# Optimization experiments

Hardware: AMD Instinct MI355X
Metric: run time of the kernel (lower is better)

## Reference

```python
import jax, jax.numpy as jnp
import numpy as np

N, K, D = 32768, 8192, 64  # active voxels, codebook size, embedding dim


def setup_inputs() -> dict:
    key = jax.random.key(0)
    k1, k2 = jax.random.split(key)
    z_feats = jax.random.normal(k1, (N, D), dtype=jnp.float32)
    codebook = jax.random.normal(k2, (K, D), dtype=jnp.float32)  # nn.Embedding weight, N(0,1)
    return {"z_feats": z_feats, "codebook": codebook}


def reference(z_feats, codebook):
    # torch.cdist(z, E) followed by argmin(dim=1). sqrt is monotonic, so argmin over
    # squared Euclidean distances gives identical indices (same math, cheaper).
    # d2[n,k] = ||z_n||^2 - 2 z_n . e_k + ||e_k||^2  -> [N, K] (dominant intermediate)
    d2 = (jnp.sum(z_feats * z_feats, axis=1, keepdims=True)
          - 2.0 * (z_feats @ codebook.T)
          + jnp.sum(codebook * codebook, axis=1))
    encoding_indices = jnp.argmin(d2, axis=1)  # [N]

    quantized_feats = codebook[encoding_indices]  # embedding gather [N, D]

    # F.mse_loss == mean over all elements
    commitment_loss = jnp.mean((z_feats - jax.lax.stop_gradient(quantized_feats)) ** 2)
    vq_loss = jnp.mean((quantized_feats - jax.lax.stop_gradient(z_feats)) ** 2)

    # straight-through estimator
    quantized = z_feats + jax.lax.stop_gradient(quantized_feats - z_feats)
    return quantized, vq_loss, commitment_loss, encoding_indices
```

## Files before the change

### kernel.cpp

```cpp
#include <hip/hip_runtime.h>
#include <cfloat>


typedef __bf16 bf16x8 __attribute__((ext_vector_type(8)));
typedef float  f32x16 __attribute__((ext_vector_type(16)));

constexpr int N_ROWS = 32768;
constexpr int K_CB   = 8192;
constexpr int D_DIM  = 64;
constexpr size_t NQ  = (size_t)N_ROWS * D_DIM;
constexpr int WS_LOSS = K_CB;
constexpr size_t WS_SPLIT_F   = 8448;
constexpr size_t SPLIT_BYTES  = (size_t)K_CB * D_DIM * 4;
constexpr size_t WS_NEED      = WS_SPLIT_F * 4 + SPLIT_BYTES;
constexpr int NROUND = K_CB / 256;

__global__ __launch_bounds__(256) void vq_prep(const float* __restrict__ cb,
                                               float* __restrict__ ws) {
  const int k = blockIdx.x * 256 + threadIdx.x;
  if (k == 0) ws[WS_LOSS] = 0.0f;
  const float4* p = reinterpret_cast<const float4*>(cb) + (size_t)k * 16;
  float s0 = 0.f, s1 = 0.f, s2 = 0.f, s3 = 0.f;
#pragma unroll
  for (int j = 0; j < 16; ++j) {
    float4 v = p[j];
    s0 = fmaf(v.x, v.x, s0); s1 = fmaf(v.y, v.y, s1);
    s2 = fmaf(v.z, v.z, s2); s3 = fmaf(v.w, v.w, s3);
  }
  ws[k] = -0.5f * ((s0 + s1) + (s2 + s3));
}

__global__ __launch_bounds__(256) void vq_split(const float* __restrict__ cb,
                                                float* __restrict__ ws) {
  const int u  = blockIdx.x * 256 + threadIdx.x;
  const int k  = u >> 3, ch = u & 7;
  const int r  = k >> 8, t = (k >> 5) & 7, c = k & 31;
  const float* src = cb + (size_t)k * D_DIM + ch * 8;
  float4 f0 = *reinterpret_cast<const float4*>(src);
  float4 f1 = *reinterpret_cast<const float4*>(src + 4);
  float xs[8] = {f0.x, f0.y, f0.z, f0.w, f1.x, f1.y, f1.z, f1.w};
  bf16x8 hi, lo;
#pragma unroll
  for (int j = 0; j < 8; ++j) {
    __bf16 h = (__bf16)xs[j];
    hi[j] = h;
    lo[j] = (__bf16)(xs[j] - (float)h);
  }
  char* base = reinterpret_cast<char*>(ws + WS_SPLIT_F) +
               (size_t)r * 65536 + (size_t)t * 8192 + (size_t)ch * 512 + (size_t)c * 16;
  *reinterpret_cast<bf16x8*>(base)        = hi;
  *reinterpret_cast<bf16x8*>(base + 4096) = lo;
}

__global__ __launch_bounds__(512, 2) void vq_gd2(const float* __restrict__ z,
                                                 const float* __restrict__ cb,
                                                 float* __restrict__ ws,
                                                 float* __restrict__ out) {
  __shared__ __attribute__((aligned(16))) unsigned char lds[12288];

  const int tid = threadIdx.x;
  const int w = tid >> 6, l = tid & 63;
  const int c = l & 31, g = l >> 5;
  const int rowbase = blockIdx.x * 128;

  bf16x8 zh[4][4], zl[4][4];
#pragma unroll
  for (int q = 0; q < 4; ++q) {
    const float* zr = z + (size_t)(rowbase + q * 32 + c) * D_DIM + 8 * g;
#pragma unroll
    for (int s = 0; s < 4; ++s) {
      float4 f0 = *reinterpret_cast<const float4*>(zr + 16 * s);
      float4 f1 = *reinterpret_cast<const float4*>(zr + 16 * s + 4);
      float xs[8] = {f0.x, f0.y, f0.z, f0.w, f1.x, f1.y, f1.z, f1.w};
#pragma unroll
      for (int j = 0; j < 8; ++j) {
        __bf16 h = (__bf16)xs[j];
        zh[q][s][j] = h;
        zl[q][s][j] = (__bf16)(xs[j] - (float)h);
      }
    }
  }

  const char* hp = reinterpret_cast<const char*>(ws + WS_SPLIT_F) +
                   (size_t)w * 8192 + (size_t)g * 512 + (size_t)c * 16;
  const char* lq = hp + 4096;
  const float* rp = ws + w * 32 + 4 * g;

  bf16x8 fh[4], fl[4];
#pragma unroll
  for (int s = 0; s < 4; ++s) {
    fh[s] = *reinterpret_cast<const bf16x8*>(hp + s * 1024);
    fl[s] = *reinterpret_cast<const bf16x8*>(lq + s * 1024);
  }
  float4 rv0 = *reinterpret_cast<const float4*>(rp);
  float4 rv1 = *reinterpret_cast<const float4*>(rp + 8);
  float4 rv2 = *reinterpret_cast<const float4*>(rp + 16);
  float4 rv3 = *reinterpret_cast<const float4*>(rp + 24);

  float gbest[4];
  int   bpack[4];
#pragma unroll
  for (int q = 0; q < 4; ++q) { gbest[q] = -FLT_MAX; bpack[q] = 0; }

  for (int r = 0; r < NROUND; ++r) {
    f32x16 ainit;
    ainit[0] = rv0.x; ainit[1] = rv0.y; ainit[2]  = rv0.z; ainit[3]  = rv0.w;
    ainit[4] = rv1.x; ainit[5] = rv1.y; ainit[6]  = rv1.z; ainit[7]  = rv1.w;
    ainit[8] = rv2.x; ainit[9] = rv2.y; ainit[10] = rv2.z; ainit[11] = rv2.w;
    ainit[12] = rv3.x; ainit[13] = rv3.y; ainit[14] = rv3.z; ainit[15] = rv3.w;
    f32x16 a0 = ainit, a1 = ainit, a2 = ainit, a3 = ainit;

    __builtin_amdgcn_s_setprio(1);
#pragma unroll
    for (int s = 0; s < 4; ++s) {
      a0 = __builtin_amdgcn_mfma_f32_32x32x16_bf16(fh[s], zh[0][s], a0, 0, 0, 0);
      a1 = __builtin_amdgcn_mfma_f32_32x32x16_bf16(fh[s], zh[1][s], a1, 0, 0, 0);
      a2 = __builtin_amdgcn_mfma_f32_32x32x16_bf16(fh[s], zh[2][s], a2, 0, 0, 0);
      a3 = __builtin_amdgcn_mfma_f32_32x32x16_bf16(fh[s], zh[3][s], a3, 0, 0, 0);
      a0 = __builtin_amdgcn_mfma_f32_32x32x16_bf16(fh[s], zl[0][s], a0, 0, 0, 0);
      a1 = __builtin_amdgcn_mfma_f32_32x32x16_bf16(fh[s], zl[1][s], a1, 0, 0, 0);
      a2 = __builtin_amdgcn_mfma_f32_32x32x16_bf16(fh[s], zl[2][s], a2, 0, 0, 0);
      a3 = __builtin_amdgcn_mfma_f32_32x32x16_bf16(fh[s], zl[3][s], a3, 0, 0, 0);
      a0 = __builtin_amdgcn_mfma_f32_32x32x16_bf16(fl[s], zh[0][s], a0, 0, 0, 0);
      a1 = __builtin_amdgcn_mfma_f32_32x32x16_bf16(fl[s], zh[1][s], a1, 0, 0, 0);
      a2 = __builtin_amdgcn_mfma_f32_32x32x16_bf16(fl[s], zh[2][s], a2, 0, 0, 0);
      a3 = __builtin_amdgcn_mfma_f32_32x32x16_bf16(fl[s], zh[3][s], a3, 0, 0, 0);
    }
    __builtin_amdgcn_s_setprio(0);

    if (r < NROUND - 1) {
      hp += 65536; lq += 65536; rp += 256;
#pragma unroll
      for (int s = 0; s < 4; ++s) {
        fh[s] = *reinterpret_cast<const bf16x8*>(hp + s * 1024);
        fl[s] = *reinterpret_cast<const bf16x8*>(lq + s * 1024);
      }
      rv0 = *reinterpret_cast<const float4*>(rp);
      rv1 = *reinterpret_cast<const float4*>(rp + 8);
      rv2 = *reinterpret_cast<const float4*>(rp + 16);
      rv3 = *reinterpret_cast<const float4*>(rp + 24);
    }

    const int pb = r << 4;
#pragma unroll
    for (int q = 0; q < 4; ++q) {
      const f32x16& a = (q == 0) ? a0 : (q == 1) ? a1 : (q == 2) ? a2 : a3;
      float m = a[0];
#pragma unroll
      for (int i = 1; i < 16; ++i) m = fmaxf(m, a[i]);
      int bi = 0;
#pragma unroll
      for (int i = 15; i >= 0; --i) bi = (a[i] == m) ? i : bi;
      bool upd = m > gbest[q];
      gbest[q] = upd ? m : gbest[q];
      bpack[q] = upd ? (pb + bi) : bpack[q];
    }
  }

  int bk[4];
#pragma unroll
  for (int q = 0; q < 4; ++q) {
    int rr = bpack[q] >> 4, i = bpack[q] & 15;
    int cid = (i & 3) + 8 * (i >> 2) + 4 * g;
    bk[q] = rr * 256 + w * 32 + cid;
  }
#pragma unroll
  for (int q = 0; q < 4; ++q) {
    float ob = __shfl_xor(gbest[q], 32, 64);
    int   ok = __shfl_xor(bk[q], 32, 64);
    if (ob > gbest[q] || (ob == gbest[q] && ok < bk[q])) { gbest[q] = ob; bk[q] = ok; }
  }

  float* fbuf = reinterpret_cast<float*>(lds);
  int*   kbuf = reinterpret_cast<int*>(lds + 4096);
  int*   ibuf = reinterpret_cast<int*>(lds + 8192);
  if (l < 32) {
#pragma unroll
    for (int q = 0; q < 4; ++q) {
      fbuf[w * 128 + q * 32 + l] = gbest[q];
      kbuf[w * 128 + q * 32 + l] = bk[q];
    }
  }
  __syncthreads();

  if (tid < 128) {
    float bb = fbuf[tid];
    int   kk = kbuf[tid];
#pragma unroll
    for (int ww = 1; ww < 8; ++ww) {
      float b2 = fbuf[ww * 128 + tid];
      int   k2 = kbuf[ww * 128 + tid];
      if (b2 > bb || (b2 == bb && k2 < kk)) { bb = b2; kk = k2; }
    }
    ibuf[tid] = kk;
    out[NQ + 2 + rowbase + tid] = (float)kk;
  }
  __syncthreads();

  {
    const int row_l = tid >> 2, seg = tid & 3;
    const int idx  = ibuf[row_l];
    const int grow = rowbase + row_l;
    const float4* qp = reinterpret_cast<const float4*>(cb + (size_t)idx * D_DIM + seg * 16);
    const float4* zp = reinterpret_cast<const float4*>(z + (size_t)grow * D_DIM + seg * 16);
    float4*       op = reinterpret_cast<float4*>(out + (size_t)grow * D_DIM + seg * 16);
    float lp = 0.f;
#pragma unroll
    for (int cc = 0; cc < 4; ++cc) {
      float4 qv = qp[cc], zv = zp[cc];
      op[cc] = qv;
      float dx = zv.x - qv.x, dy = zv.y - qv.y;
      float dz = zv.z - qv.z, dw = zv.w - qv.w;
      lp += (dx * dx + dy * dy) + (dz * dz + dw * dw);
    }
#pragma unroll
    for (int off = 32; off > 0; off >>= 1) lp += __shfl_down(lp, off, 64);
    if (l == 0) atomicAdd(ws + WS_LOSS, lp);
  }
}

__global__ __launch_bounds__(512, 2) void vq_main_reg(const float* __restrict__ z,
                                                      const float* __restrict__ cb,
                                                      float* __restrict__ ws,
                                                      float* __restrict__ out) {
  __shared__ __attribute__((aligned(16))) unsigned char lds[65536];
  const int tid = threadIdx.x;
  const int w = tid >> 6, l = tid & 63;
  const int rg = w >> 1, sp = w & 1;
  const int c = l & 31, g = l >> 5;
  const int rowbase = blockIdx.x * 128;
  const int myrow = rowbase + rg * 32 + c;

  bf16x8 zh[4], zl[4];
#pragma unroll
  for (int s = 0; s < 4; ++s) {
    const float* zp = z + (size_t)myrow * D_DIM + 16 * s + 8 * g;
    float4 f0 = *reinterpret_cast<const float4*>(zp);
    float4 f1 = *reinterpret_cast<const float4*>(zp + 4);
    float xs[8] = {f0.x, f0.y, f0.z, f0.w, f1.x, f1.y, f1.z, f1.w};
#pragma unroll
    for (int j = 0; j < 8; ++j) {
      __bf16 h = (__bf16)xs[j];
      zh[s][j] = h; zl[s][j] = (__bf16)(xs[j] - (float)h);
    }
  }
  const int st_t01 = tid >> 8;
  const int st_c   = (tid >> 3) & 31;
  const int st_ch  = tid & 7;
  const unsigned st_off = (unsigned)(st_t01 * 16384 + st_ch * 512 + st_c * 16);
  const float* st_g = cb + (size_t)(st_t01 * 32 + st_c) * D_DIM + st_ch * 8;

  float best = -FLT_MAX;
  int   bidx = 0;
  float4 p0 = *reinterpret_cast<const float4*>(st_g);
  float4 p1 = *reinterpret_cast<const float4*>(st_g + 4);
  {
    float xs[8] = {p0.x, p0.y, p0.z, p0.w, p1.x, p1.y, p1.z, p1.w};
    bf16x8 hi, lo;
#pragma unroll
    for (int j = 0; j < 8; ++j) {
      __bf16 h = (__bf16)xs[j];
      hi[j] = h; lo[j] = (__bf16)(xs[j] - (float)h);
    }
    *reinterpret_cast<bf16x8*>(lds + st_off)        = hi;
    *reinterpret_cast<bf16x8*>(lds + st_off + 8192) = lo;
  }
  __syncthreads();
  const unsigned rd_base = (unsigned)(sp * 16384 + c * 16);
  for (int r = 0; r < 128; ++r) {
    const int buf = r & 1;
    if (r < 127) {
      const float* gp = st_g + (size_t)(r + 1) * (64 * D_DIM);
      p0 = *reinterpret_cast<const float4*>(gp);
      p1 = *reinterpret_cast<const float4*>(gp + 4);
    }
    const unsigned b0 = (unsigned)buf * 32768u + rd_base;
    bf16x8 ch[4], cl[4];
#pragma unroll
    for (int s = 0; s < 4; ++s) {
      unsigned off = b0 + (unsigned)((2 * s + g) * 512);
      ch[s] = *reinterpret_cast<const bf16x8*>(lds + off);
      cl[s] = *reinterpret_cast<const bf16x8*>(lds + off + 8192);
    }
    f32x16 acc;
#pragma unroll
    for (int i = 0; i < 16; ++i) acc[i] = 0.f;
#pragma unroll
    for (int s = 0; s < 4; ++s) {
      acc = __builtin_amdgcn_mfma_f32_32x32x16_bf16(ch[s], zh[s], acc, 0, 0, 0);
      acc = __builtin_amdgcn_mfma_f32_32x32x16_bf16(ch[s], zl[s], acc, 0, 0, 0);
      acc = __builtin_amdgcn_mfma_f32_32x32x16_bf16(cl[s], zh[s], acc, 0, 0, 0);
    }
    const int tb = (2 * r + sp) * 32 + 4 * g;
#pragma unroll
    for (int q = 0; q < 4; ++q) {
      float4 rv = *reinterpret_cast<const float4*>(ws + tb + 8 * q);
      float ra[4] = {rv.x, rv.y, rv.z, rv.w};
#pragma unroll
      for (int j = 0; j < 4; ++j) {
        float sc = ra[j] + acc[4 * q + j];
        int kg = tb + 8 * q + j;
        if (sc > best) { best = sc; bidx = kg; }
      }
    }
    if (r < 127) {
      float xs[8] = {p0.x, p0.y, p0.z, p0.w, p1.x, p1.y, p1.z, p1.w};
      bf16x8 hi, lo;
#pragma unroll
      for (int j = 0; j < 8; ++j) {
        __bf16 h = (__bf16)xs[j];
        hi[j] = h; lo[j] = (__bf16)(xs[j] - (float)h);
      }
      unsigned wo = (unsigned)(buf ^ 1) * 32768u + st_off;
      *reinterpret_cast<bf16x8*>(lds + wo)        = hi;
      *reinterpret_cast<bf16x8*>(lds + wo + 8192) = lo;
    }
    __syncthreads();
  }
  {
    float ob = __shfl_xor(best, 32, 64);
    int   oi = __shfl_xor(bidx, 32, 64);
    if (ob > best || (ob == best && oi < bidx)) { best = ob; bidx = oi; }
  }
  float* mf  = reinterpret_cast<float*>(lds);
  int*   mi  = reinterpret_cast<int*>(lds + 1024);
  int*   mix = reinterpret_cast<int*>(lds + 2048);
  if (l < 32) { mf[w * 32 + c] = best; mi[w * 32 + c] = bidx; }
  __syncthreads();
  if (tid < 128) {
    int rgg = tid >> 5, rl = tid & 31;
    float b0 = mf[(2 * rgg) * 32 + rl];     int i0 = mi[(2 * rgg) * 32 + rl];
    float b1 = mf[(2 * rgg + 1) * 32 + rl]; int i1 = mi[(2 * rgg + 1) * 32 + rl];
    int idx = (b1 > b0 || (b1 == b0 && i1 < i0)) ? i1 : i0;
    mix[tid] = idx;
    out[NQ + 2 + rowbase + tid] = (float)idx;
  }
  __syncthreads();
  {
    const int row_l = tid >> 2, seg = tid & 3;
    const int idx  = mix[row_l];
    const int grow = rowbase + row_l;
    const float4* qp = reinterpret_cast<const float4*>(cb + (size_t)idx * D_DIM + seg * 16);
    const float4* zp = reinterpret_cast<const float4*>(z + (size_t)grow * D_DIM + seg * 16);
    float4*       op = reinterpret_cast<float4*>(out + (size_t)grow * D_DIM + seg * 16);
    float lp = 0.f;
#pragma unroll
    for (int cc = 0; cc < 4; ++cc) {
      float4 qv = qp[cc], zv = zp[cc];
      op[cc] = qv;
      float dx = zv.x - qv.x, dy = zv.y - qv.y;
      float dz = zv.z - qv.z, dw = zv.w - qv.w;
      lp += (dx * dx + dy * dy) + (dz * dz + dw * dw);
    }
#pragma unroll
    for (int off = 32; off > 0; off >>= 1) lp += __shfl_down(lp, off, 64);
    if (l == 0) atomicAdd(ws + WS_LOSS, lp);
  }
}

__global__ void vq_fin(const float* __restrict__ ws, float* __restrict__ out) {
  float mm = ws[WS_LOSS] * (1.0f / (float)(N_ROWS * D_DIM));
  out[NQ]     = mm;
  out[NQ + 1] = mm;
}

extern "C" void kernel_launch(void* const* d_in, const int* in_sizes, int n_in,
                              void* d_out, int out_size, void* d_ws, size_t ws_size,
                              hipStream_t stream) {
  (void)in_sizes; (void)n_in; (void)out_size;
  const float* z  = (const float*)d_in[0];
  const float* cb = (const float*)d_in[1];
  float* out = (float*)d_out;
  float* ws  = (float*)d_ws;

  vq_prep<<<K_CB / 256, 256, 0, stream>>>(cb, ws);
  if (ws_size >= WS_NEED) {
    vq_split<<<256, 256, 0, stream>>>(cb, ws);
    vq_gd2<<<N_ROWS / 128, 512, 0, stream>>>(z, cb, ws, out);
  } else {
    vq_main_reg<<<N_ROWS / 128, 512, 0, stream>>>(z, cb, ws, out);
  }
  vq_fin<<<1, 1, 0, stream>>>(ws, out);
}
```

Measured before the change: 129.4 us.

## Halve rows per block to raise occupancy in VQ distance kernel

The fused distance/argmin kernel now processes 64 rows per block instead of 128, keeping two MFMA accumulators per wave and launching twice as many blocks with a min-blocks hint of 4. Lower register pressure and a larger grid are meant to improve latency hiding and CU fill. In exchange, each codebook fragment loaded from global memory is reused across half as many rows, doubling codebook read traffic. The epilogue reduction and gather are resized to match.

```diff
diff --git a/kernel.cpp b/kernel.cpp
--- a/kernel.cpp
+++ b/kernel.cpp
@@ -52,20 +52,20 @@
   *reinterpret_cast<bf16x8*>(base + 4096) = lo;
 }
 
-__global__ __launch_bounds__(512, 2) void vq_gd2(const float* __restrict__ z,
+__global__ __launch_bounds__(512, 4) void vq_gd3(const float* __restrict__ z,
                                                  const float* __restrict__ cb,
                                                  float* __restrict__ ws,
                                                  float* __restrict__ out) {
-  __shared__ __attribute__((aligned(16))) unsigned char lds[12288];
+  __shared__ __attribute__((aligned(16))) unsigned char lds[8192];
 
   const int tid = threadIdx.x;
   const int w = tid >> 6, l = tid & 63;
   const int c = l & 31, g = l >> 5;
-  const int rowbase = blockIdx.x * 128;
-
-  bf16x8 zh[4][4], zl[4][4];
-#pragma unroll
-  for (int q = 0; q < 4; ++q) {
+  const int rowbase = blockIdx.x * 64;
+
+  bf16x8 zh[2][4], zl[2][4];
+#pragma unroll
+  for (int q = 0; q < 2; ++q) {
     const float* zr = z + (size_t)(rowbase + q * 32 + c) * D_DIM + 8 * g;
 #pragma unroll
     for (int s = 0; s < 4; ++s) {
@@ -97,34 +97,26 @@
   float4 rv2 = *reinterpret_cast<const float4*>(rp + 16);
   float4 rv3 = *reinterpret_cast<const float4*>(rp + 24);
 
-  float gbest[4];
-  int   bpack[4];
-#pragma unroll
-  for (int q = 0; q < 4; ++q) { gbest[q] = -FLT_MAX; bpack[q] = 0; }
+  float gbest0 = -FLT_MAX, gbest1 = -FLT_MAX;
+  int   bp0 = 0, bp1 = 0;
 
   for (int r = 0; r < NROUND; ++r) {
     f32x16 ainit;
-    ainit[0] = rv0.x; ainit[1] = rv0.y; ainit[2]  = rv0.z; ainit[3]  = rv0.w;
-    ainit[4] = rv1.x; ainit[5] = rv1.y; ainit[6]  = rv1.z; ainit[7]  = rv1.w;
-    ainit[8] = rv2.x; ainit[9] = rv2.y; ainit[10] = rv2.z; ainit[11] = rv2.w;
+    ainit[0]  = rv0.x; ainit[1]  = rv0.y; ainit[2]  = rv0.z; ainit[3]  = rv0.w;
+    ainit[4]  = rv1.x; ainit[5]  = rv1.y; ainit[6]  = rv1.z; ainit[7]  = rv1.w;
+    ainit[8]  = rv2.x; ainit[9]  = rv2.y; ainit[10] = rv2.z; ainit[11] = rv2.w;
     ainit[12] = rv3.x; ainit[13] = rv3.y; ainit[14] = rv3.z; ainit[15] = rv3.w;
-    f32x16 a0 = ainit, a1 = ainit, a2 = ainit, a3 = ainit;
+    f32x16 a0 = ainit, a1 = ainit;
 
     __builtin_amdgcn_s_setprio(1);
 #pragma unroll
     for (int s = 0; s < 4; ++s) {
       a0 = __builtin_amdgcn_mfma_f32_32x32x16_bf16(fh[s], zh[0][s], a0, 0, 0, 0);
       a1 = __builtin_amdgcn_mfma_f32_32x32x16_bf16(fh[s], zh[1][s], a1, 0, 0, 0);
-      a2 = __builtin_amdgcn_mfma_f32_32x32x16_bf16(fh[s], zh[2][s], a2, 0, 0, 0);
-      a3 = __builtin_amdgcn_mfma_f32_32x32x16_bf16(fh[s], zh[3][s], a3, 0, 0, 0);
       a0 = __builtin_amdgcn_mfma_f32_32x32x16_bf16(fh[s], zl[0][s], a0, 0, 0, 0);
       a1 = __builtin_amdgcn_mfma_f32_32x32x16_bf16(fh[s], zl[1][s], a1, 0, 0, 0);
-      a2 = __builtin_amdgcn_mfma_f32_32x32x16_bf16(fh[s], zl[2][s], a2, 0, 0, 0);
-      a3 = __builtin_amdgcn_mfma_f32_32x32x16_bf16(fh[s], zl[3][s], a3, 0, 0, 0);
       a0 = __builtin_amdgcn_mfma_f32_32x32x16_bf16(fl[s], zh[0][s], a0, 0, 0, 0);
       a1 = __builtin_amdgcn_mfma_f32_32x32x16_bf16(fl[s], zh[1][s], a1, 0, 0, 0);
-      a2 = __builtin_amdgcn_mfma_f32_32x32x16_bf16(fl[s], zh[2][s], a2, 0, 0, 0);
-      a3 = __builtin_amdgcn_mfma_f32_32x32x16_bf16(fl[s], zh[3][s], a3, 0, 0, 0);
     }
     __builtin_amdgcn_s_setprio(0);
 
@@ -142,54 +134,62 @@
     }
 
     const int pb = r << 4;
-#pragma unroll
-    for (int q = 0; q < 4; ++q) {
-      const f32x16& a = (q == 0) ? a0 : (q == 1) ? a1 : (q == 2) ? a2 : a3;
-      float m = a[0];
-#pragma unroll
-      for (int i = 1; i < 16; ++i) m = fmaxf(m, a[i]);
+    {
+      float m = a0[0];
+#pragma unroll
+      for (int i = 1; i < 16; ++i) m = fmaxf(m, a0[i]);
       int bi = 0;
 #pragma unroll
-      for (int i = 15; i >= 0; --i) bi = (a[i] == m) ? i : bi;
-      bool upd = m > gbest[q];
-      gbest[q] = upd ? m : gbest[q];
-      bpack[q] = upd ? (pb + bi) : bpack[q];
-    }
-  }
-
-  int bk[4];
-#pragma unroll
-  for (int q = 0; q < 4; ++q) {
-    int rr = bpack[q] >> 4, i = bpack[q] & 15;
-    int cid = (i & 3) + 8 * (i >> 2) + 4 * g;
-    bk[q] = rr * 256 + w * 32 + cid;
-  }
-#pragma unroll
-  for (int q = 0; q < 4; ++q) {
-    float ob = __shfl_xor(gbest[q], 32, 64);
-    int   ok = __shfl_xor(bk[q], 32, 64);
-    if (ob > gbest[q] || (ob == gbest[q] && ok < bk[q])) { gbest[q] = ob; bk[q] = ok; }
+      for (int i = 15; i >= 0; --i) bi = (a0[i] == m) ? i : bi;
+      bool upd = m > gbest0;
+      gbest0 = upd ? m : gbest0;
+      bp0    = upd ? (pb + bi) : bp0;
+    }
+    {
+      float m = a1[0];
+#pragma unroll
+      for (int i = 1; i < 16; ++i) m = fmaxf(m, a1[i]);
+      int bi = 0;
+#pragma unroll
+      for (int i = 15; i >= 0; --i) bi = (a1[i] == m) ? i : bi;
+      bool upd = m > gbest1;
+      gbest1 = upd ? m : gbest1;
+      bp1    = upd ? (pb + bi) : bp1;
+    }
+  }
+
+  int bk0, bk1;
+  {
+    int rr = bp0 >> 4, i = bp0 & 15;
+    bk0 = rr * 256 + w * 32 + (i & 3) + 8 * (i >> 2) + 4 * g;
+    rr = bp1 >> 4; i = bp1 & 15;
+    bk1 = rr * 256 + w * 32 + (i & 3) + 8 * (i >> 2) + 4 * g;
+  }
+  {
+    float ob = __shfl_xor(gbest0, 32, 64);
+    int   ok = __shfl_xor(bk0, 32, 64);
+    if (ob > gbest0 || (ob == gbest0 && ok < bk0)) { gbest0 = ob; bk0 = ok; }
+    ob = __shfl_xor(gbest1, 32, 64);
+    ok = __shfl_xor(bk1, 32, 64);
+    if (ob > gbest1 || (ob == gbest1 && ok < bk1)) { gbest1 = ob; bk1 = ok; }
   }
 
   float* fbuf = reinterpret_cast<float*>(lds);
-  int*   kbuf = reinterpret_cast<int*>(lds + 4096);
-  int*   ibuf = reinterpret_cast<int*>(lds + 8192);
+  int*   kbuf = reinterpret_cast<int*>(lds + 2048);
+  int*   ibuf = reinterpret_cast<int*>(lds + 4096);
   if (l < 32) {
-#pragma unroll
-    for (int q = 0; q < 4; ++q) {
-      fbuf[w * 128 + q * 32 + l] = gbest[q];
-      kbuf[w * 128 + q * 32 + l] = bk[q];
-    }
-  }
-  __syncthreads();
-
-  if (tid < 128) {
+    fbuf[w * 64 + c]      = gbest0;  kbuf[w * 64 + c]      = bk0;
+    fbuf[w * 64 + 32 + c] = gbest1;  kbuf[w * 64 + 32 + c] = bk1;
+  }
+  __syncthreads();
+
+  if (tid < 64) {
     float bb = fbuf[tid];
     int   kk = kbuf[tid];
 #pragma unroll
     for (int ww = 1; ww < 8; ++ww) {
-      float b2 = fbuf[ww * 128 + tid];
-      int   k2 = kbuf[ww * 128 + tid];
+      float b2 = fbuf[ww * 64 + tid];
+      int   k2 = kbuf[ww * 64 + tid];
       if (b2 > bb || (b2 == bb && k2 < kk)) { bb = b2; kk = k2; }
     }
     ibuf[tid] = kk;
@@ -198,15 +198,15 @@
   __syncthreads();
 
   {
-    const int row_l = tid >> 2, seg = tid & 3;
+    const int row_l = tid >> 3, seg = tid & 7;
     const int idx  = ibuf[row_l];
     const int grow = rowbase + row_l;
-    const float4* qp = reinterpret_cast<const float4*>(cb + (size_t)idx * D_DIM + seg * 16);
-    const float4* zp = reinterpret_cast<const float4*>(z + (size_t)grow * D_DIM + seg * 16);
-    float4*       op = reinterpret_cast<float4*>(out + (size_t)grow * D_DIM + seg * 16);
+    const float4* qp = reinterpret_cast<const float4*>(cb + (size_t)idx * D_DIM + seg * 8);
+    const float4* zp = reinterpret_cast<const float4*>(z + (size_t)grow * D_DIM + seg * 8);
+    float4*       op = reinterpret_cast<float4*>(out + (size_t)grow * D_DIM + seg * 8);
     float lp = 0.f;
 #pragma unroll
-    for (int cc = 0; cc < 4; ++cc) {
+    for (int cc = 0; cc < 2; ++cc) {
       float4 qv = qp[cc], zv = zp[cc];
       op[cc] = qv;
       float dx = zv.x - qv.x, dy = zv.y - qv.y;
@@ -376,7 +376,7 @@
   vq_prep<<<K_CB / 256, 256, 0, stream>>>(cb, ws);
   if (ws_size >= WS_NEED) {
     vq_split<<<256, 256, 0, stream>>>(cb, ws);
-    vq_gd2<<<N_ROWS / 128, 512, 0, stream>>>(z, cb, ws, out);
+    vq_gd3<<<N_ROWS / 64, 512, 0, stream>>>(z, cb, ws, out);
   } else {
     vq_main_reg<<<N_ROWS / 128, 512, 0, stream>>>(z, cb, ws, out);
   }
```

Result: slower. 215.4 us (+66.4%).

## Process two codebook tiles per wave per round with eight accumulators

Applied to the files above, without the earlier changes.

Each wave now handles 64 codebook entries per round instead of 32, running 16 rounds with eight 32x32 accumulators. The split-codebook layout becomes a flat per-tile layout, the codebook fragments are loaded inside the MFMA loop rather than prefetched a round ahead, and the argmax bookkeeping encodes the extra tile bit. The intent is to halve the per-round loop and epilogue overhead relative to MFMA work. The cost is higher register pressure: launch_bounds drops the min-2-blocks hint, so occupancy may fall, and the explicit prefetch and setprio are gone.

```diff
diff --git a/kernel.cpp b/kernel.cpp
--- a/kernel.cpp
+++ b/kernel.cpp
@@ -13,7 +13,10 @@
 constexpr size_t WS_SPLIT_F   = 8448;
 constexpr size_t SPLIT_BYTES  = (size_t)K_CB * D_DIM * 4;
 constexpr size_t WS_NEED      = WS_SPLIT_F * 4 + SPLIT_BYTES;
-constexpr int NROUND = K_CB / 256;
+
+static __device__ __forceinline__ f32x16 MF(bf16x8 a, bf16x8 b, f32x16 c) {
+  return __builtin_amdgcn_mfma_f32_32x32x16_bf16(a, b, c, 0, 0, 0);
+}
 
 __global__ __launch_bounds__(256) void vq_prep(const float* __restrict__ cb,
                                                float* __restrict__ ws) {
@@ -34,7 +37,7 @@
                                                 float* __restrict__ ws) {
   const int u  = blockIdx.x * 256 + threadIdx.x;
   const int k  = u >> 3, ch = u & 7;
-  const int r  = k >> 8, t = (k >> 5) & 7, c = k & 31;
+  const int tile = k >> 5, c = k & 31;
   const float* src = cb + (size_t)k * D_DIM + ch * 8;
   float4 f0 = *reinterpret_cast<const float4*>(src);
   float4 f1 = *reinterpret_cast<const float4*>(src + 4);
@@ -47,15 +50,15 @@
     lo[j] = (__bf16)(xs[j] - (float)h);
   }
   char* base = reinterpret_cast<char*>(ws + WS_SPLIT_F) +
-               (size_t)r * 65536 + (size_t)t * 8192 + (size_t)ch * 512 + (size_t)c * 16;
+               (size_t)tile * 8192 + (size_t)ch * 512 + (size_t)c * 16;
   *reinterpret_cast<bf16x8*>(base)        = hi;
   *reinterpret_cast<bf16x8*>(base + 4096) = lo;
 }
 
-__global__ __launch_bounds__(512, 2) void vq_gd2(const float* __restrict__ z,
-                                                 const float* __restrict__ cb,
-                                                 float* __restrict__ ws,
-                                                 float* __restrict__ out) {
+__global__ __launch_bounds__(512) void vq_c8(const float* __restrict__ z,
+                                             const float* __restrict__ cb,
+                                             float* __restrict__ ws,
+                                             float* __restrict__ out) {
   __shared__ __attribute__((aligned(16))) unsigned char lds[12288];
 
   const int tid = threadIdx.x;
@@ -81,88 +84,92 @@
     }
   }
 
-  const char* hp = reinterpret_cast<const char*>(ws + WS_SPLIT_F) +
-                   (size_t)w * 8192 + (size_t)g * 512 + (size_t)c * 16;
-  const char* lq = hp + 4096;
-  const float* rp = ws + w * 32 + 4 * g;
-
-  bf16x8 fh[4], fl[4];
-#pragma unroll
-  for (int s = 0; s < 4; ++s) {
-    fh[s] = *reinterpret_cast<const bf16x8*>(hp + s * 1024);
-    fl[s] = *reinterpret_cast<const bf16x8*>(lq + s * 1024);
-  }
-  float4 rv0 = *reinterpret_cast<const float4*>(rp);
-  float4 rv1 = *reinterpret_cast<const float4*>(rp + 8);
-  float4 rv2 = *reinterpret_cast<const float4*>(rp + 16);
-  float4 rv3 = *reinterpret_cast<const float4*>(rp + 24);
+  const char*  cbbase = reinterpret_cast<const char*>(ws + WS_SPLIT_F) +
+                        (size_t)(2 * w) * 8192 + (size_t)g * 512 + (size_t)c * 16;
+  const float* rbase  = ws + w * 64 + 4 * g;
 
   float gbest[4];
   int   bpack[4];
 #pragma unroll
   for (int q = 0; q < 4; ++q) { gbest[q] = -FLT_MAX; bpack[q] = 0; }
 
-  for (int r = 0; r < NROUND; ++r) {
-    f32x16 ainit;
-    ainit[0] = rv0.x; ainit[1] = rv0.y; ainit[2]  = rv0.z; ainit[3]  = rv0.w;
-    ainit[4] = rv1.x; ainit[5] = rv1.y; ainit[6]  = rv1.z; ainit[7]  = rv1.w;
-    ainit[8] = rv2.x; ainit[9] = rv2.y; ainit[10] = rv2.z; ainit[11] = rv2.w;
-    ainit[12] = rv3.x; ainit[13] = rv3.y; ainit[14] = rv3.z; ainit[15] = rv3.w;
-    f32x16 a0 = ainit, a1 = ainit, a2 = ainit, a3 = ainit;
-
-    __builtin_amdgcn_s_setprio(1);
+  f32x16 a00, a01, a02, a03, a10, a11, a12, a13;
+
+  for (int r = 0; r < 16; ++r) {
+    {
+      const float* rp = rbase + r * 512;
+      float4 p0 = *reinterpret_cast<const float4*>(rp);
+      float4 p1 = *reinterpret_cast<const float4*>(rp + 8);
+      float4 p2 = *reinterpret_cast<const float4*>(rp + 16);
+      float4 p3 = *reinterpret_cast<const float4*>(rp + 24);
+      float4 p4 = *reinterpret_cast<const float4*>(rp + 32);
+      float4 p5 = *reinterpret_cast<const float4*>(rp + 40);
+      float4 p6 = *reinterpret_cast<const float4*>(rp + 48);
+      float4 p7 = *reinterpret_cast<const float4*>(rp + 56);
+      f32x16 i0, i1;
+      i0[0] = p0.x; i0[1] = p0.y; i0[2]  = p0.z; i0[3]  = p0.w;
+      i0[4] = p1.x; i0[5] = p1.y; i0[6]  = p1.z; i0[7]  = p1.w;
+      i0[8] = p2.x; i0[9] = p2.y; i0[10] = p2.z; i0[11] = p2.w;
+      i0[12] = p3.x; i0[13] = p3.y; i0[14] = p3.z; i0[15] = p3.w;
+      i1[0] = p4.x; i1[1] = p4.y; i1[2]  = p4.z; i1[3]  = p4.w;
+      i1[4] = p5.x; i1[5] = p5.y; i1[6]  = p5.z; i1[7]  = p5.w;
+      i1[8] = p6.x; i1[9] = p6.y; i1[10] = p6.z; i1[11] = p6.w;
+      i1[12] = p7.x; i1[13] = p7.y; i1[14] = p7.z; i1[15] = p7.w;
+      a00 = i0; a01 = i0; a02 = i0; a03 = i0;
+      a10 = i1; a11 = i1; a12 = i1; a13 = i1;
+    }
+
+    const char* cb_ = cbbase + (size_t)r * 131072;
 #pragma unroll
     for (int s = 0; s < 4; ++s) {
-      a0 = __builtin_amdgcn_mfma_f32_32x32x16_bf16(fh[s], zh[0][s], a0, 0, 0, 0);
-      a1 = __builtin_amdgcn_mfma_f32_32x32x16_bf16(fh[s], zh[1][s], a1, 0, 0, 0);
-      a2 = __builtin_amdgcn_mfma_f32_32x32x16_bf16(fh[s], zh[2][s], a2, 0, 0, 0);
-      a3 = __builtin_amdgcn_mfma_f32_32x32x16_bf16(fh[s], zh[3][s], a3, 0, 0, 0);
-      a0 = __builtin_amdgcn_mfma_f32_32x32x16_bf16(fh[s], zl[0][s], a0, 0, 0, 0);
-      a1 = __builtin_amdgcn_mfma_f32_32x32x16_bf16(fh[s], zl[1][s], a1, 0, 0, 0);
-      a2 = __builtin_amdgcn_mfma_f32_32x32x16_bf16(fh[s], zl[2][s], a2, 0, 0, 0);
-      a3 = __builtin_amdgcn_mfma_f32_32x32x16_bf16(fh[s], zl[3][s], a3, 0, 0, 0);
-      a0 = __builtin_amdgcn_mfma_f32_32x32x16_bf16(fl[s], zh[0][s], a0, 0, 0, 0);
-      a1 = __builtin_amdgcn_mfma_f32_32x32x16_bf16(fl[s], zh[1][s], a1, 0, 0, 0);
-      a2 = __builtin_amdgcn_mfma_f32_32x32x16_bf16(fl[s], zh[2][s], a2, 0, 0, 0);
-      a3 = __builtin_amdgcn_mfma_f32_32x32x16_bf16(fl[s], zh[3][s], a3, 0, 0, 0);
-    }
-    __builtin_amdgcn_s_setprio(0);
-
-    if (r < NROUND - 1) {
-      hp += 65536; lq += 65536; rp += 256;
-#pragma unroll
-      for (int s = 0; s < 4; ++s) {
-        fh[s] = *reinterpret_cast<const bf16x8*>(hp + s * 1024);
-        fl[s] = *reinterpret_cast<const bf16x8*>(lq + s * 1024);
-      }
-      rv0 = *reinterpret_cast<const float4*>(rp);
-      rv1 = *reinterpret_cast<const float4*>(rp + 8);
-      rv2 = *reinterpret_cast<const float4*>(rp + 16);
-      rv3 = *reinterpret_cast<const float4*>(rp + 24);
-    }
-
-    const int pb = r << 4;
-#pragma unroll
-    for (int q = 0; q < 4; ++q) {
-      const f32x16& a = (q == 0) ? a0 : (q == 1) ? a1 : (q == 2) ? a2 : a3;
-      float m = a[0];
-#pragma unroll
-      for (int i = 1; i < 16; ++i) m = fmaxf(m, a[i]);
-      int bi = 0;
-#pragma unroll
-      for (int i = 15; i >= 0; --i) bi = (a[i] == m) ? i : bi;
-      bool upd = m > gbest[q];
-      gbest[q] = upd ? m : gbest[q];
-      bpack[q] = upd ? (pb + bi) : bpack[q];
-    }
+      bf16x8 fh0 = *reinterpret_cast<const bf16x8*>(cb_ + s * 1024);
+      bf16x8 fl0 = *reinterpret_cast<const bf16x8*>(cb_ + 4096 + s * 1024);
+      bf16x8 fh1 = *reinterpret_cast<const bf16x8*>(cb_ + 8192 + s * 1024);
+      bf16x8 fl1 = *reinterpret_cast<const bf16x8*>(cb_ + 12288 + s * 1024);
+      a00 = MF(fh0, zh[0][s], a00); a01 = MF(fh0, zh[1][s], a01);
+      a02 = MF(fh0, zh[2][s], a02); a03 = MF(fh0, zh[3][s], a03);
+      a10 = MF(fh1, zh[0][s], a10); a11 = MF(fh1, zh[1][s], a11);
+      a12 = MF(fh1, zh[2][s], a12); a13 = MF(fh1, zh[3][s], a13);
+      a00 = MF(fh0, zl[0][s], a00); a01 = MF(fh0, zl[1][s], a01);
+      a02 = MF(fh0, zl[2][s], a02); a03 = MF(fh0, zl[3][s], a03);
+      a10 = MF(fh1, zl[0][s], a10); a11 = MF(fh1, zl[1][s], a11);
+      a12 = MF(fh1, zl[2][s], a12); a13 = MF(fh1, zl[3][s], a13);
+      a00 = MF(fl0, zh[0][s], a00); a01 = MF(fl0, zh[1][s], a01);
+      a02 = MF(fl0, zh[2][s], a02); a03 = MF(fl0, zh[3][s], a03);
+      a10 = MF(fl1, zh[0][s], a10); a11 = MF(fl1, zh[1][s], a11);
+      a12 = MF(fl1, zh[2][s], a12); a13 = MF(fl1, zh[3][s], a13);
+    }
+
+#define EPI1(ACC, GB, BP, PB)                                                  \
+    do {                                                                       \
+      float m_ = ACC[0];                                                       \
+      _Pragma("unroll")                                                        \
+      for (int i = 1; i < 16; ++i) m_ = fmaxf(m_, ACC[i]);                     \
+      int bi_ = 0;                                                             \
+      _Pragma("unroll")                                                        \
+      for (int i = 15; i >= 0; --i) bi_ = (ACC[i] == m_) ? i : bi_;            \
+      if (m_ > GB) { GB = m_; BP = (PB) + bi_; }                               \
+    } while (0)
+
+    const int pb0 = (r << 5);
+    const int pb1 = (r << 5) | 16;
+    EPI1(a00, gbest[0], bpack[0], pb0);
+    EPI1(a01, gbest[1], bpack[1], pb0);
+    EPI1(a02, gbest[2], bpack[2], pb0);
+    EPI1(a03, gbest[3], bpack[3], pb0);
+    EPI1(a10, gbest[0], bpack[0], pb1);
+    EPI1(a11, gbest[1], bpack[1], pb1);
+    EPI1(a12, gbest[2], bpack[2], pb1);
+    EPI1(a13, gbest[3], bpack[3], pb1);
+#undef EPI1
   }
 
   int bk[4];
 #pragma unroll
   for (int q = 0; q < 4; ++q) {
-    int rr = bpack[q] >> 4, i = bpack[q] & 15;
+    int rr = bpack[q] >> 5, tt = (bpack[q] >> 4) & 1, i = bpack[q] & 15;
     int cid = (i & 3) + 8 * (i >> 2) + 4 * g;
-    bk[q] = rr * 256 + w * 32 + cid;
+    bk[q] = rr * 512 + w * 64 + tt * 32 + cid;
   }
 #pragma unroll
   for (int q = 0; q < 4; ++q) {
@@ -376,7 +383,7 @@
   vq_prep<<<K_CB / 256, 256, 0, stream>>>(cb, ws);
   if (ws_size >= WS_NEED) {
     vq_split<<<256, 256, 0, stream>>>(cb, ws);
-    vq_gd2<<<N_ROWS / 128, 512, 0, stream>>>(z, cb, ws, out);
+    vq_c8<<<N_ROWS / 128, 512, 0, stream>>>(z, cb, ws, out);
   } else {
     vq_main_reg<<<N_ROWS / 128, 512, 0, stream>>>(z, cb, ws, out);
   }
```

Result: slower. 149.8 us (+15.8%).
